# Optimization experiments

Measured on AMD Instinct MI355X. Metric: run time of the kernel, lower is better.

Reference implementation:

```python
import jax, jax.numpy as jnp
import numpy as np

REFSIZE = 1024  # init kwarg refsize -> self.N
EPS = float(np.finfo(np.float32).eps)


def interp1d(x, y, xnew):
    """Batched linear interpolation, faithful to Interp1d.forward.
    x, y: (D, N) with x sorted along last dim; xnew: (D, P). Returns (D, P)."""
    # torch.searchsorted default (right=False) == numpy/jnp side='left'
    ind = jax.vmap(jnp.searchsorted)(x, xnew) - 1
    ind = jnp.clip(ind, 0, x.shape[1] - 2)
    slopes = (y[:, 1:] - y[:, :-1]) / (EPS + (x[:, 1:] - x[:, :-1]))
    x_sel = jnp.take_along_axis(x, ind, axis=1)
    y_sel = jnp.take_along_axis(y, ind, axis=1)
    s_sel = jnp.take_along_axis(slopes, ind, axis=1)
    return y_sel + s_sel * (xnew - x_sel)


def setup_inputs() -> dict:
    key = jax.random.key(0)
    k1, k2 = jax.random.split(key)
    l, n = 2048, 4096
    x1 = jax.random.uniform(k1, (l, n), dtype=jnp.float32)  # points on [0,1)
    w = jax.random.uniform(k2, (l, n), dtype=jnp.float32)
    x1_weights = w / jnp.sum(w, axis=-1, keepdims=True)  # row-normalized masses
    return {"x1": x1, "x1_weights": x1_weights}


def reference(x1, x1_weights):
    l, n = x1.shape
    N = REFSIZE
    ref = jnp.linspace(0.0, 1.0, N + 1, dtype=jnp.float32)[:-1]  # (N,)

    # empirical_cdf: sort samples, cumsum weights
    order = jnp.argsort(x1, axis=-1)
    xs = jnp.take_along_axis(x1, order, axis=-1)          # (l, n) sorted samples
    ys = jnp.cumsum(jnp.take_along_axis(x1_weights, order, axis=-1), axis=-1)  # CDF

    # emb
    alpha = (jnp.sum(x1 * x1_weights, axis=-1) / jnp.sum(x1_weights, axis=-1) - 0.5)[:, None]
    xnew = jnp.broadcast_to(jnp.linspace(-1.0, 2.0, 3 * N, dtype=jnp.float32)[None, :], (l, 3 * N))
    int_x = jnp.floor(xnew)
    rest_x = xnew - int_x
    ecdf = int_x + interp1d(xs, ys, rest_x)               # (l, 3N) extended CDF

    x_grid = jnp.broadcast_to(ref[None, :], (l, N))
    embedd = interp1d(ecdf, xnew, x_grid - alpha) - x_grid  # inverse-CDF embedding

    # circular cost
    a = jnp.abs(embedd)
    m = jnp.minimum(a, 1.0 - a)
    return jnp.sqrt(jnp.mean(jnp.sum(m * m, axis=-1)) + 1e-8)
```

## Files before the change

kernel.cpp:

```cpp
#include <hip/hip_runtime.h>
#include <math.h>

#define L    2048
#define NCOL 4096
#define NG   1024
#define N3   3072
#define T    512
#define NW   8
#define EPT  8
#define NB   2048
#define FEPS 1.1920929e-07f

typedef unsigned long long u64;
typedef unsigned short u16;
typedef unsigned int u32;

__device__ __forceinline__ int lower_bound_f(const float* a, int lo, int hi, float v) {
  while (lo < hi) {
    int mid = (lo + hi) >> 1;
    if (a[mid] < v) lo = mid + 1; else hi = mid;
  }
  return lo;
}

__device__ __forceinline__ int bucket_of_bits(unsigned xb) {
  float f = __uint_as_float(xb);
  int b = (int)(f * (float)NB);
  return b > NB - 1 ? NB - 1 : b;
}

__device__ __forceinline__ int swz(int i) { return i ^ ((i >> 5) & 7); }

__global__ __launch_bounds__(T, 8) void lcot_rows(const float* __restrict__ X,
                                                  const float* __restrict__ W,
                                                  float* __restrict__ rowsum) {
  extern __shared__ char smem[];
  u64*   pairs = (u64*)smem;
  float* xs    = (float*)smem;
  float* wy    = (float*)(smem + 16384);
  float* ecdf  = (float*)(smem + 16384);
  u16*   cnt16 = (u16*)(smem + 32768);
  u32*   cntw  = (u32*)(smem + 32768);

  __shared__ float redA[NW], redB[NW], fwt[NW];
  __shared__ int   iwt[NW];
  __shared__ float s_alpha;

  const int tid  = threadIdx.x;
  const int lane = tid & 63;
  const int wave = tid >> 6;
  const int row  = blockIdx.x;
  const float* xr = X + (size_t)row * NCOL;
  const float* wr = W + (size_t)row * NCOL;

  for (int i = tid; i < 1025; i += T) cntw[i] = 0u;

  u64 key[EPT];
  float sxw = 0.f, sw = 0.f;
  const float4* xr4 = (const float4*)xr;
  const float4* wr4 = (const float4*)wr;
#pragma unroll
  for (int c = 0; c < 2; ++c) {
    float4 xv = xr4[tid * 2 + c];
    float4 ww = wr4[tid * 2 + c];
    sxw += xv.x * ww.x + xv.y * ww.y + xv.z * ww.z + xv.w * ww.w;
    sw  += ww.x + ww.y + ww.z + ww.w;
    int b = 8 * tid + 4 * c;
    key[4*c+0] = ((u64)__float_as_uint(xv.x) << 32) | (unsigned)(b + 0);
    key[4*c+1] = ((u64)__float_as_uint(xv.y) << 32) | (unsigned)(b + 1);
    key[4*c+2] = ((u64)__float_as_uint(xv.z) << 32) | (unsigned)(b + 2);
    key[4*c+3] = ((u64)__float_as_uint(xv.w) << 32) | (unsigned)(b + 3);
  }
#pragma unroll
  for (int off = 32; off > 0; off >>= 1) {
    sxw += __shfl_down(sxw, off);
    sw  += __shfl_down(sw, off);
  }
  if (lane == 0) { redA[wave] = sxw; redB[wave] = sw; }
  __syncthreads();

  u32 bo[EPT];
#pragma unroll
  for (int e = 0; e < EPT; ++e) {
    int b = bucket_of_bits((unsigned)(key[e] >> 32));
    u32 inc = (b & 1) ? 65536u : 1u;
    u32 ret = atomicAdd(&cntw[b >> 1], inc);
    u32 o = (b & 1) ? (ret >> 16) : (ret & 0xffffu);
    bo[e] = ((u32)b << 16) | (o & 0xffffu);
  }
  __syncthreads();
  if (tid == 0) {
    float a = 0.f, b = 0.f;
#pragma unroll
    for (int i = 0; i < NW; ++i) { a += redA[i]; b += redB[i]; }
    s_alpha = a / b - 0.5f;
  }

  u32 cv0 = cntw[2 * tid], cv1 = cntw[2 * tid + 1];
  int c0 = (int)(cv0 & 0xffffu), c1 = (int)(cv0 >> 16);
  int c2 = (int)(cv1 & 0xffffu), c3 = (int)(cv1 >> 16);
  int runi = c0 + c1 + c2 + c3;
  int toti = runi, prei = runi;
#pragma unroll
  for (int off = 1; off < 64; off <<= 1) {
    int v = __shfl_up(prei, off);
    if (lane >= off) prei += v;
  }
  if (lane == 63) iwt[wave] = prei;
  __syncthreads();
  int wpre = 0;
#pragma unroll
  for (int w2 = 0; w2 < NW; ++w2) wpre += (w2 < wave) ? iwt[w2] : 0;
  int acc = wpre + prei - toti;
  {
    int b0 = acc; acc += c0;
    int b1 = acc; acc += c1;
    int b2 = acc; acc += c2;
    int b3 = acc; acc += c3;
    cntw[2 * tid]     = (u32)b0 | ((u32)b1 << 16);
    cntw[2 * tid + 1] = (u32)b2 | ((u32)b3 << 16);
  }
  if (tid == T - 1) cnt16[NB] = (u16)acc;
  __syncthreads();

#pragma unroll
  for (int e = 0; e < EPT; ++e) {
    int b = (int)(bo[e] >> 16);
    int o = (int)(bo[e] & 0xffffu);
    pairs[(int)cnt16[b] + o] = key[e];
  }
  __syncthreads();

#pragma unroll
  for (int bb = 0; bb < 4; ++bb) {
    int b  = 4 * tid + bb;
    int lo = (int)cnt16[b], hi = (int)cnt16[b + 1];
    int n = hi - lo;
    if (n >= 2) {
      int hm1 = hi - 1;
      u64 e0 = pairs[lo];
      u64 e1 = pairs[lo + 1];
      u64 t2 = pairs[lo + 2 < hm1 ? lo + 2 : hm1];
      u64 t3 = pairs[lo + 3 < hm1 ? lo + 3 : hm1];
      u64 e2 = (n > 2) ? t2 : ~0ull;
      u64 e3 = (n > 3) ? t3 : ~0ull;
      { u64 a = e0 < e1 ? e0 : e1; e1 = e0 < e1 ? e1 : e0; e0 = a; }
      { u64 a = e2 < e3 ? e2 : e3; e3 = e2 < e3 ? e3 : e2; e2 = a; }
      { u64 a = e0 < e2 ? e0 : e2; e2 = e0 < e2 ? e2 : e0; e0 = a; }
      { u64 a = e1 < e3 ? e1 : e3; e3 = e1 < e3 ? e3 : e1; e1 = a; }
      { u64 a = e1 < e2 ? e1 : e2; e2 = e1 < e2 ? e2 : e1; e1 = a; }
      pairs[lo]     = e0;
      pairs[lo + 1] = e1;
      if (n > 2) pairs[lo + 2] = e2;
      if (n > 3) pairs[lo + 3] = e3;
      for (int i = lo + 4; i < hi; ++i) {
        u64 v = pairs[i];
        int j = i - 1;
        while (j >= lo && pairs[j] > v) { pairs[j + 1] = pairs[j]; --j; }
        pairs[j + 1] = v;
      }
    }
  }
  __syncthreads();

  u64 q[EPT];
#pragma unroll
  for (int m = 0; m < EPT; ++m) q[m] = pairs[tid + m * T];
  float wg[EPT];
#pragma unroll
  for (int m = 0; m < EPT; ++m) wg[m] = wr[(u32)(q[m] & 0xffffffffu)];
  __syncthreads();

#pragma unroll
  for (int m = 0; m < EPT; ++m) {
    int j = tid + m * T;
    xs[j]      = __uint_as_float((u32)(q[m] >> 32));
    wy[swz(j)] = wg[m];
  }
  __syncthreads();

  float lw[EPT];
  float runf = 0.f;
#pragma unroll
  for (int c = 0; c < EPT; ++c) {
    runf += wy[swz(8 * tid + c)];
    lw[c] = runf;
  }
  float totf = runf, pref = runf;
#pragma unroll
  for (int off = 1; off < 64; off <<= 1) {
    float v = __shfl_up(pref, off);
    if (lane >= off) pref += v;
  }
  if (lane == 63) fwt[wave] = pref;
  __syncthreads();
  float wpf = 0.f;
#pragma unroll
  for (int w2 = 0; w2 < NW; ++w2) wpf += (w2 < wave) ? fwt[w2] : 0.f;
  float basef = wpf + pref - totf;
#pragma unroll
  for (int c = 0; c < EPT; ++c) wy[swz(8 * tid + c)] = basef + lw[c];
  __syncthreads();

  float ev[N3 / T];
#pragma unroll
  for (int g = 0; g < 2; ++g) {
    int lo0, hi0, lo1, hi1, lo2, hi2;
    float r0, r1, r2;
    {
      int j = tid + (3 * g + 0) * T;
      float xnew = -1.0f + (3.0f * (float)j) / 3071.0f;
      r0 = xnew - floorf(xnew);
      int k = (int)(r0 * (float)NB); k = k > NB - 1 ? NB - 1 : k;
      lo0 = (int)cnt16[k]; hi0 = (int)cnt16[k + 1];
    }
    {
      int j = tid + (3 * g + 1) * T;
      float xnew = -1.0f + (3.0f * (float)j) / 3071.0f;
      r1 = xnew - floorf(xnew);
      int k = (int)(r1 * (float)NB); k = k > NB - 1 ? NB - 1 : k;
      lo1 = (int)cnt16[k]; hi1 = (int)cnt16[k + 1];
    }
    {
      int j = tid + (3 * g + 2) * T;
      float xnew = -1.0f + (3.0f * (float)j) / 3071.0f;
      r2 = xnew - floorf(xnew);
      int k = (int)(r2 * (float)NB); k = k > NB - 1 ? NB - 1 : k;
      lo2 = (int)cnt16[k]; hi2 = (int)cnt16[k + 1];
    }
    while ((lo0 < hi0) | (lo1 < hi1) | (lo2 < hi2)) {
      if (lo0 < hi0) { int m = (lo0 + hi0) >> 1; if (xs[m] < r0) lo0 = m + 1; else hi0 = m; }
      if (lo1 < hi1) { int m = (lo1 + hi1) >> 1; if (xs[m] < r1) lo1 = m + 1; else hi1 = m; }
      if (lo2 < hi2) { int m = (lo2 + hi2) >> 1; if (xs[m] < r2) lo2 = m + 1; else hi2 = m; }
    }
#pragma unroll
    for (int s3 = 0; s3 < 3; ++s3) {
      int s = 3 * g + s3;
      int lb = (s3 == 0) ? lo0 : (s3 == 1) ? lo1 : lo2;
      float rest = (s3 == 0) ? r0 : (s3 == 1) ? r1 : r2;
      int j = tid + s * T;
      float xnew = -1.0f + (3.0f * (float)j) / 3071.0f;
      float ix = floorf(xnew);
      int ind = lb - 1;
      ind = ind < 0 ? 0 : (ind > NCOL - 2 ? NCOL - 2 : ind);
      float x0 = xs[ind], x1v = xs[ind + 1];
      float y0 = wy[swz(ind)], y1v = wy[swz(ind + 1)];
      float slope = (y1v - y0) * __builtin_amdgcn_rcpf(FEPS + (x1v - x0));
      ev[s] = ix + (y0 + slope * (rest - x0));
    }
  }
  __syncthreads();

#pragma unroll
  for (int s = 0; s < N3 / T; ++s) ecdf[tid + s * T] = ev[s];
  __syncthreads();

  float alpha = s_alpha;
  float accf = 0.f;
  {
    float xg0 = (float)tid / 1024.0f;
    float xg1 = (float)(tid + T) / 1024.0f;
    float q0 = xg0 - alpha;
    float q1 = xg1 - alpha;
    int lo0 = 0, hi0 = N3, lo1 = 0, hi1 = N3;
    while ((lo0 < hi0) | (lo1 < hi1)) {
      if (lo0 < hi0) { int m = (lo0 + hi0) >> 1; if (ecdf[m] < q0) lo0 = m + 1; else hi0 = m; }
      if (lo1 < hi1) { int m = (lo1 + hi1) >> 1; if (ecdf[m] < q1) lo1 = m + 1; else hi1 = m; }
    }
#pragma unroll
    for (int s = 0; s < 2; ++s) {
      int lo = (s == 0) ? lo0 : lo1;
      float q2 = (s == 0) ? q0 : q1;
      float xg = (s == 0) ? xg0 : xg1;
      int ind = lo - 1;
      ind = ind < 0 ? 0 : (ind > N3 - 2 ? N3 - 2 : ind);
      float e0 = ecdf[ind], e1 = ecdf[ind + 1];
      float y0 = -1.0f + (3.0f * (float)ind) / 3071.0f;
      float y1 = -1.0f + (3.0f * (float)(ind + 1)) / 3071.0f;
      float slope = (y1 - y0) * __builtin_amdgcn_rcpf(FEPS + (e1 - e0));
      float emb = y0 + slope * (q2 - e0) - xg;
      float a = fabsf(emb);
      float m = fminf(a, 1.0f - a);
      accf += m * m;
    }
  }
#pragma unroll
  for (int off = 32; off > 0; off >>= 1) accf += __shfl_down(accf, off);
  if (lane == 0) redA[wave] = accf;
  __syncthreads();
  if (tid == 0) {
    float s = 0.f;
#pragma unroll
    for (int i = 0; i < NW; ++i) s += redA[i];
    rowsum[row] = s;
  }
}

__global__ __launch_bounds__(256) void lcot_final(const float* __restrict__ rowsum,
                                                  float* __restrict__ out) {
  __shared__ float red[4];
  int t = threadIdx.x;
  float s = 0.f;
  for (int i = t; i < L; i += 256) s += rowsum[i];
#pragma unroll
  for (int off = 32; off > 0; off >>= 1) s += __shfl_down(s, off);
  if ((t & 63) == 0) red[t >> 6] = s;
  __syncthreads();
  if (t == 0) {
    float tot = red[0] + red[1] + red[2] + red[3];
    out[0] = sqrtf(tot / (float)L + 1e-8f);
  }
}

extern "C" void kernel_launch(void* const* d_in, const int* in_sizes, int n_in,
                              void* d_out, int out_size, void* d_ws, size_t ws_size,
                              hipStream_t stream) {
  const float* X = (const float*)d_in[0];
  const float* W = (const float*)d_in[1];
  float* rowsum = (float*)d_ws;
  size_t shbytes = 32768 + 4104;
  hipLaunchKernelGGL(lcot_rows, dim3(L), dim3(T), shbytes, stream, X, W, rowsum);
  hipLaunchKernelGGL(lcot_final, dim3(1), dim3(256), 0, stream,
                     (const float*)rowsum, (float*)d_out);
}
```

Before: 179.8 us.

## Keep sorted pairs in place, fuse CDF into pairs, add LUT for inverse search

The sorted (x, index) pairs are now stored under an XOR swizzle and reused in place. The low word of each pair is overwritten with the cumulative weight, which removes the separate xs/wy arrays along with a scatter pass and a barrier. Interpolation loads x and y together as one 64-bit value. A 257-entry lookup table over the ecdf range narrows the second binary search, at the cost of an extra table build, an extra barrier and a bit more shared memory.

New measurement: 183.8 us. 2.2% more time.

```diff
diff --git a/kernel.cpp b/kernel.cpp
--- a/kernel.cpp
+++ b/kernel.cpp
@@ -29,18 +29,23 @@
   return b > NB - 1 ? NB - 1 : b;
 }
 
-__device__ __forceinline__ int swz(int i) { return i ^ ((i >> 5) & 7); }
+__device__ __forceinline__ int P_(int i) { return i ^ ((i >> 4) & 15); }
+__device__ __forceinline__ u64 prd(const u64* p, int i) { return p[P_(i)]; }
+__device__ __forceinline__ void pwr(u64* p, int i, u64 v) { p[P_(i)] = v; }
+__device__ __forceinline__ float xhi(const u32* pw, int i) {
+  return __uint_as_float(pw[2 * P_(i) + 1]);
+}
 
 __global__ __launch_bounds__(T, 8) void lcot_rows(const float* __restrict__ X,
                                                   const float* __restrict__ W,
                                                   float* __restrict__ rowsum) {
   extern __shared__ char smem[];
   u64*   pairs = (u64*)smem;
-  float* xs    = (float*)smem;
-  float* wy    = (float*)(smem + 16384);
-  float* ecdf  = (float*)(smem + 16384);
+  u32*   pw    = (u32*)smem;
+  float* ecdf  = (float*)smem;
   u16*   cnt16 = (u16*)(smem + 32768);
   u32*   cntw  = (u32*)(smem + 32768);
+  u16*   lut2  = (u16*)(smem + 36872);
 
   __shared__ float redA[NW], redB[NW], fwt[NW];
   __shared__ int   iwt[NW];
@@ -127,7 +132,7 @@
   for (int e = 0; e < EPT; ++e) {
     int b = (int)(bo[e] >> 16);
     int o = (int)(bo[e] & 0xffffu);
-    pairs[(int)cnt16[b] + o] = key[e];
+    pwr(pairs, (int)cnt16[b] + o, key[e]);
   }
   __syncthreads();
 
@@ -138,10 +143,10 @@
     int n = hi - lo;
     if (n >= 2) {
       int hm1 = hi - 1;
-      u64 e0 = pairs[lo];
-      u64 e1 = pairs[lo + 1];
-      u64 t2 = pairs[lo + 2 < hm1 ? lo + 2 : hm1];
-      u64 t3 = pairs[lo + 3 < hm1 ? lo + 3 : hm1];
+      u64 e0 = prd(pairs, lo);
+      u64 e1 = prd(pairs, lo + 1);
+      u64 t2 = prd(pairs, lo + 2 < hm1 ? lo + 2 : hm1);
+      u64 t3 = prd(pairs, lo + 3 < hm1 ? lo + 3 : hm1);
       u64 e2 = (n > 2) ? t2 : ~0ull;
       u64 e3 = (n > 3) ? t3 : ~0ull;
       { u64 a = e0 < e1 ? e0 : e1; e1 = e0 < e1 ? e1 : e0; e0 = a; }
@@ -149,15 +154,15 @@
       { u64 a = e0 < e2 ? e0 : e2; e2 = e0 < e2 ? e2 : e0; e0 = a; }
       { u64 a = e1 < e3 ? e1 : e3; e3 = e1 < e3 ? e3 : e1; e1 = a; }
       { u64 a = e1 < e2 ? e1 : e2; e2 = e1 < e2 ? e2 : e1; e1 = a; }
-      pairs[lo]     = e0;
-      pairs[lo + 1] = e1;
-      if (n > 2) pairs[lo + 2] = e2;
-      if (n > 3) pairs[lo + 3] = e3;
-      for (int i = lo + 4; i < hi; ++i) {
-        u64 v = pairs[i];
-        int j = i - 1;
-        while (j >= lo && pairs[j] > v) { pairs[j + 1] = pairs[j]; --j; }
-        pairs[j + 1] = v;
+      pwr(pairs, lo,     e0);
+      pwr(pairs, lo + 1, e1);
+      if (n > 2) pwr(pairs, lo + 2, e2);
+      if (n > 3) pwr(pairs, lo + 3, e3);
+      for (int i2 = lo + 4; i2 < hi; ++i2) {
+        u64 v = prd(pairs, i2);
+        int j = i2 - 1;
+        while (j >= lo && prd(pairs, j) > v) { pwr(pairs, j + 1, prd(pairs, j)); --j; }
+        pwr(pairs, j + 1, v);
       }
     }
   }
@@ -165,27 +170,14 @@
 
   u64 q[EPT];
 #pragma unroll
-  for (int m = 0; m < EPT; ++m) q[m] = pairs[tid + m * T];
+  for (int c = 0; c < EPT; ++c) q[c] = prd(pairs, 8 * tid + c);
   float wg[EPT];
 #pragma unroll
-  for (int m = 0; m < EPT; ++m) wg[m] = wr[(u32)(q[m] & 0xffffffffu)];
-  __syncthreads();
-
-#pragma unroll
-  for (int m = 0; m < EPT; ++m) {
-    int j = tid + m * T;
-    xs[j]      = __uint_as_float((u32)(q[m] >> 32));
-    wy[swz(j)] = wg[m];
-  }
-  __syncthreads();
-
+  for (int c = 0; c < EPT; ++c) wg[c] = wr[(u32)(q[c] & 0xffffffffu)];
   float lw[EPT];
   float runf = 0.f;
 #pragma unroll
-  for (int c = 0; c < EPT; ++c) {
-    runf += wy[swz(8 * tid + c)];
-    lw[c] = runf;
-  }
+  for (int c = 0; c < EPT; ++c) { runf += wg[c]; lw[c] = runf; }
   float totf = runf, pref = runf;
 #pragma unroll
   for (int off = 1; off < 64; off <<= 1) {
@@ -199,7 +191,8 @@
   for (int w2 = 0; w2 < NW; ++w2) wpf += (w2 < wave) ? fwt[w2] : 0.f;
   float basef = wpf + pref - totf;
 #pragma unroll
-  for (int c = 0; c < EPT; ++c) wy[swz(8 * tid + c)] = basef + lw[c];
+  for (int c = 0; c < EPT; ++c)
+    pw[2 * P_(8 * tid + c)] = __float_as_uint(basef + lw[c]);
   __syncthreads();
 
   float ev[N3 / T];
@@ -229,9 +222,9 @@
       lo2 = (int)cnt16[k]; hi2 = (int)cnt16[k + 1];
     }
     while ((lo0 < hi0) | (lo1 < hi1) | (lo2 < hi2)) {
-      if (lo0 < hi0) { int m = (lo0 + hi0) >> 1; if (xs[m] < r0) lo0 = m + 1; else hi0 = m; }
-      if (lo1 < hi1) { int m = (lo1 + hi1) >> 1; if (xs[m] < r1) lo1 = m + 1; else hi1 = m; }
-      if (lo2 < hi2) { int m = (lo2 + hi2) >> 1; if (xs[m] < r2) lo2 = m + 1; else hi2 = m; }
+      if (lo0 < hi0) { int m = (lo0 + hi0) >> 1; if (xhi(pw, m) < r0) lo0 = m + 1; else hi0 = m; }
+      if (lo1 < hi1) { int m = (lo1 + hi1) >> 1; if (xhi(pw, m) < r1) lo1 = m + 1; else hi1 = m; }
+      if (lo2 < hi2) { int m = (lo2 + hi2) >> 1; if (xhi(pw, m) < r2) lo2 = m + 1; else hi2 = m; }
     }
 #pragma unroll
     for (int s3 = 0; s3 < 3; ++s3) {
@@ -243,8 +236,12 @@
       float ix = floorf(xnew);
       int ind = lb - 1;
       ind = ind < 0 ? 0 : (ind > NCOL - 2 ? NCOL - 2 : ind);
-      float x0 = xs[ind], x1v = xs[ind + 1];
-      float y0 = wy[swz(ind)], y1v = wy[swz(ind + 1)];
+      u64 v0 = prd(pairs, ind);
+      u64 v1 = prd(pairs, ind + 1);
+      float x0  = __uint_as_float((u32)(v0 >> 32));
+      float y0  = __uint_as_float((u32)(v0 & 0xffffffffu));
+      float x1v = __uint_as_float((u32)(v1 >> 32));
+      float y1v = __uint_as_float((u32)(v1 & 0xffffffffu));
       float slope = (y1v - y0) * __builtin_amdgcn_rcpf(FEPS + (x1v - x0));
       ev[s] = ix + (y0 + slope * (rest - x0));
     }
@@ -253,6 +250,12 @@
 
 #pragma unroll
   for (int s = 0; s < N3 / T; ++s) ecdf[tid + s * T] = ev[s];
+  __syncthreads();
+
+  if (tid < 257) {
+    float v = -1.0f + 3.0f * (float)tid * (1.0f / 256.0f);
+    lut2[tid] = (u16)lower_bound_f(ecdf, 0, N3, v);
+  }
   __syncthreads();
 
   float alpha = s_alpha;
@@ -262,7 +265,14 @@
     float xg1 = (float)(tid + T) / 1024.0f;
     float q0 = xg0 - alpha;
     float q1 = xg1 - alpha;
-    int lo0 = 0, hi0 = N3, lo1 = 0, hi1 = N3;
+    int k20 = (int)floorf((q0 + 1.0f) * (256.0f / 3.0f));
+    int k21 = (int)floorf((q1 + 1.0f) * (256.0f / 3.0f));
+    k20 = k20 < 0 ? 0 : (k20 > 255 ? 255 : k20);
+    k21 = k21 < 0 ? 0 : (k21 > 255 ? 255 : k21);
+    int lo0 = (int)lut2[k20 > 0 ? k20 - 1 : 0];
+    int hi0 = (int)lut2[k20 < 254 ? k20 + 2 : 256];
+    int lo1 = (int)lut2[k21 > 0 ? k21 - 1 : 0];
+    int hi1 = (int)lut2[k21 < 254 ? k21 + 2 : 256];
     while ((lo0 < hi0) | (lo1 < hi1)) {
       if (lo0 < hi0) { int m = (lo0 + hi0) >> 1; if (ecdf[m] < q0) lo0 = m + 1; else hi0 = m; }
       if (lo1 < hi1) { int m = (lo1 + hi1) >> 1; if (ecdf[m] < q1) lo1 = m + 1; else hi1 = m; }
@@ -318,7 +328,7 @@
   const float* X = (const float*)d_in[0];
   const float* W = (const float*)d_in[1];
   float* rowsum = (float*)d_ws;
-  size_t shbytes = 32768 + 4104;
+  size_t shbytes = 32768 + 4104 + 520;
   hipLaunchKernelGGL(lcot_rows, dim3(L), dim3(T), shbytes, stream, X, W, rowsum);
   hipLaunchKernelGGL(lcot_final, dim3(1), dim3(256), 0, stream,
                      (const float*)rowsum, (float*)d_out);
```
